# Kernel tuning notes

Hardware: AMD Instinct MI355X
Metric: run time of the kernel (lower is better)

Reference implementation:

```python
import jax, jax.numpy as jnp
import numpy as np

NEG_SLOPE = 0.01  # nn.LeakyReLU default


def setup_inputs() -> dict:
    key = jax.random.key(0)
    k1, k2, k3, k4, k5, k6 = jax.random.split(key, 6)
    N, E, F_IN, F_OUT = 50000, 800000, 256, 64
    x = jax.random.normal(k1, (N, F_IN), dtype=jnp.float32)
    src = jax.random.randint(k2, (E,), 0, N, dtype=jnp.int32)
    dst = jax.random.randint(k3, (E,), 0, N, dtype=jnp.int32)
    # nn.init.normal_(weight, 0, 0.5) for both Linear layers (no bias)
    W1 = 0.5 * jax.random.normal(k4, (F_OUT, F_IN), dtype=jnp.float32)
    W2 = 0.5 * jax.random.normal(k5, (F_OUT, F_OUT), dtype=jnp.float32)
    # detGAT.a = torch.rand(2*out_feats, 1)
    a = jax.random.uniform(k6, (2 * F_OUT, 1), dtype=jnp.float32)
    return {"x": x, "W1": W1, "W2": W2, "a": a, "src": src, "dst": dst}


def reference(x, W1, W2, a, src, dst):
    N, d = x.shape[0], W1.shape[0]
    # model_base: linear -> (dropout, identity in eval) -> relu, twice
    z = jax.nn.relu(x @ W1.T)
    h = jax.nn.relu(z @ W2.T)  # [N, d]
    # detGAT edge score: LeakyReLU(concat([h_dst, h_src]) @ a)
    # split a so we compute per-node dot products once instead of an [E, 2d] concat
    a_dst, a_src = a[:d, 0], a[d:, 0]
    s_dst = h @ a_dst  # [N]
    s_src = h @ a_src  # [N]
    score = jax.nn.leaky_relu(s_dst[dst] + s_src[src], NEG_SLOPE)  # [E]
    # edge_softmax: softmax over incoming edges of each destination node
    m = jax.ops.segment_max(score, dst, num_segments=N)  # [N]
    e = jnp.exp(score - m[dst])
    ssum = jax.ops.segment_sum(e, dst, num_segments=N)  # [N]
    w = e / ssum[dst]  # [E]
    # weighted scatter-sum of src features to dst nodes
    res = jax.ops.segment_sum(h[src] * w[:, None], dst, num_segments=N)  # [N, d]
    return jax.nn.relu(h - res)
```

## Files before the change

### kernel.cpp

```cpp
#include <hip/hip_runtime.h>
#include <math.h>

#define F_IN 256
#define F_OUT 64
#define NEG_SLOPE 0.01f
#define CAP 8192
#define NB2 256

typedef unsigned short ushort8_t __attribute__((ext_vector_type(8)));
typedef __bf16 bf16x8 __attribute__((ext_vector_type(8)));
typedef float f32x16 __attribute__((ext_vector_type(16)));

__device__ inline unsigned short f2bf(float f) {
    unsigned u = __float_as_uint(f);
    u += 0x7FFF + ((u >> 16) & 1);
    return (unsigned short)(u >> 16);
}
__device__ inline float bf2f(unsigned short u) {
    return __uint_as_float(((unsigned)u) << 16);
}
__device__ inline void splitbf(float x, unsigned short& hi, unsigned short& lo) {
    hi = f2bf(x);
    lo = f2bf(x - bf2f(hi));
}
__device__ inline bf16x8 asbf8(ushort8_t u) {
    union { ushort8_t u; bf16x8 b; } c; c.u = u; return c.b;
}
__device__ inline float redq32(float v) {
    v += __shfl_xor(v, 1);  v += __shfl_xor(v, 2);  v += __shfl_xor(v, 4);
    v += __shfl_xor(v, 8);  v += __shfl_xor(v, 16);
    return v;
}

__global__ __launch_bounds__(1024)
void prep_scatter_kernel(const float* __restrict__ W1, const float* __restrict__ W2,
                         unsigned short* __restrict__ w1fh, unsigned short* __restrict__ w1fl,
                         unsigned short* __restrict__ w2fh, unsigned short* __restrict__ w2fl,
                         const int* __restrict__ src, const int* __restrict__ dst,
                         int* __restrict__ cursor, int* __restrict__ edata,
                         int E, int chunk)
{
    __shared__ int lh[256], lbase[256], lcur[256];
    const int tid = threadIdx.x;

    if (blockIdx.x < 16) {
        int idx = blockIdx.x * 1024 + tid;
        int jj = idx & 7, l = (idx >> 3) & 63, t = idx >> 9;
        {
            int nt = t & 1, gks = t >> 1;
            int f = nt * 32 + (l & 31);
            int k = gks * 16 + (l >> 5) * 8 + jj;
            unsigned short hi, lo;
            splitbf(W1[f * F_IN + k], hi, lo);
            w1fh[idx] = hi; w1fl[idx] = lo;
        }
        if (idx < 4096) {
            int nt = t & 1, ks = t >> 1;
            int f = nt * 32 + (l & 31);
            int j = ks * 16 + (l >> 5) * 8 + jj;
            unsigned short hi, lo;
            splitbf(W2[f * F_OUT + j], hi, lo);
            w2fh[idx] = hi; w2fl[idx] = lo;
        }
        return;
    }

    const int bid = blockIdx.x - 16;
    if (tid < 256) lh[tid] = 0;
    __syncthreads();
    const int beg = bid * chunk;
    const int end = min(E, beg + chunk);
    for (int i = beg + tid; i < end; i += 1024)
        atomicAdd(&lh[((unsigned)dst[i]) >> 8], 1);
    __syncthreads();
    if (tid < 256) {
        int c = lh[tid];
        lbase[tid] = c ? atomicAdd(&cursor[tid], c) : 0;
        lcur[tid] = 0;
    }
    __syncthreads();
    for (int i = beg + tid; i < end; i += 1024) {
        int d = dst[i];
        int s = src[i];
        int b = ((unsigned)d) >> 8;
        int rk = atomicAdd(&lcur[b], 1);
        edata[b * CAP + lbase[b] + rk] = ((d & 0xFF) << 16) | s;
    }
}

__global__ __launch_bounds__(256, 2)
void mlp_kernel(const float* __restrict__ x,
                const unsigned short* __restrict__ w1fh,
                const unsigned short* __restrict__ w1fl,
                const unsigned short* __restrict__ w2fh,
                const unsigned short* __restrict__ w2fl,
                const float* __restrict__ a,
                unsigned short* __restrict__ hb,
                float* __restrict__ sdst,
                float* __restrict__ ssrc, int N)
{
    __shared__ __align__(16) unsigned short zbuf[4 * 8576];

    const int tid = threadIdx.x;
    const int lane = tid & 63;
    const int wid = __builtin_amdgcn_readfirstlane(tid >> 6);
    const int ml = lane & 31;
    const int q = lane >> 5;
    const int hl = lane >> 5;
    const int cl = lane & 31;
    const int node0w = blockIdx.x * 128 + wid * 32;

    unsigned short* xh = zbuf + wid * 8576;
    unsigned short* xl = xh + 4288;
    unsigned short* zh = xh;
    unsigned short* zl = xh + 2112;

    f32x16 acc0, acc1;
#pragma unroll
    for (int i = 0; i < 16; i++) { acc0[i] = 0.f; acc1[i] = 0.f; }

#pragma unroll
    for (int half = 0; half < 2; half++) {
        float4 v[16];
#pragma unroll
        for (int i = 0; i < 16; i++) {
            int r = 2 * i + hl;
            int rr = min(node0w + r, N - 1);
            v[i] = *(const float4*)(x + (size_t)rr * F_IN + half * 128 + cl * 4);
        }
#pragma unroll
        for (int i = 0; i < 16; i++) {
            int r = 2 * i + hl;
            ushort4 h4, l4;
            unsigned short th, tl;
            splitbf(v[i].x, th, tl); h4.x = th; l4.x = tl;
            splitbf(v[i].y, th, tl); h4.y = th; l4.y = tl;
            splitbf(v[i].z, th, tl); h4.z = th; l4.z = tl;
            splitbf(v[i].w, th, tl); h4.w = th; l4.w = tl;
            *(ushort4*)(xh + r * 134 + cl * 4) = h4;
            *(ushort4*)(xl + r * 134 + cl * 4) = l4;
        }
#pragma unroll
        for (int ks = 0; ks < 8; ks++) {
            int gks = half * 8 + ks;
            bf16x8 ah = asbf8(*(const ushort8_t*)(xh + ml * 134 + ks * 16 + q * 8));
            bf16x8 al = asbf8(*(const ushort8_t*)(xl + ml * 134 + ks * 16 + q * 8));
            bf16x8 bh0 = asbf8(*(const ushort8_t*)(w1fh + ((gks * 2 + 0) * 64 + lane) * 8));
            bf16x8 bl0 = asbf8(*(const ushort8_t*)(w1fl + ((gks * 2 + 0) * 64 + lane) * 8));
            bf16x8 bh1 = asbf8(*(const ushort8_t*)(w1fh + ((gks * 2 + 1) * 64 + lane) * 8));
            bf16x8 bl1 = asbf8(*(const ushort8_t*)(w1fl + ((gks * 2 + 1) * 64 + lane) * 8));
            acc0 = __builtin_amdgcn_mfma_f32_32x32x16_bf16(ah, bh0, acc0, 0, 0, 0);
            acc0 = __builtin_amdgcn_mfma_f32_32x32x16_bf16(ah, bl0, acc0, 0, 0, 0);
            acc0 = __builtin_amdgcn_mfma_f32_32x32x16_bf16(al, bh0, acc0, 0, 0, 0);
            acc1 = __builtin_amdgcn_mfma_f32_32x32x16_bf16(ah, bh1, acc1, 0, 0, 0);
            acc1 = __builtin_amdgcn_mfma_f32_32x32x16_bf16(ah, bl1, acc1, 0, 0, 0);
            acc1 = __builtin_amdgcn_mfma_f32_32x32x16_bf16(al, bh1, acc1, 0, 0, 0);
        }
    }

#pragma unroll
    for (int reg = 0; reg < 16; reg++) {
        int nd = (reg & 3) + 8 * (reg >> 2) + 4 * q;
        float z0 = fmaxf(acc0[reg], 0.f);
        float z1 = fmaxf(acc1[reg], 0.f);
        unsigned short h_, l_;
        splitbf(z0, h_, l_);
        zh[nd * 66 + ml] = h_; zl[nd * 66 + ml] = l_;
        splitbf(z1, h_, l_);
        zh[nd * 66 + 32 + ml] = h_; zl[nd * 66 + 32 + ml] = l_;
    }

    f32x16 hacc0, hacc1;
#pragma unroll
    for (int i = 0; i < 16; i++) { hacc0[i] = 0.f; hacc1[i] = 0.f; }
#pragma unroll
    for (int ks = 0; ks < 4; ks++) {
        bf16x8 wh0 = asbf8(*(const ushort8_t*)(w2fh + ((ks * 2 + 0) * 64 + lane) * 8));
        bf16x8 wl0 = asbf8(*(const ushort8_t*)(w2fl + ((ks * 2 + 0) * 64 + lane) * 8));
        bf16x8 wh1 = asbf8(*(const ushort8_t*)(w2fh + ((ks * 2 + 1) * 64 + lane) * 8));
        bf16x8 wl1 = asbf8(*(const ushort8_t*)(w2fl + ((ks * 2 + 1) * 64 + lane) * 8));
        bf16x8 ah = asbf8(*(const ushort8_t*)(zh + ml * 66 + ks * 16 + q * 8));
        bf16x8 al = asbf8(*(const ushort8_t*)(zl + ml * 66 + ks * 16 + q * 8));
        hacc0 = __builtin_amdgcn_mfma_f32_32x32x16_bf16(ah, wh0, hacc0, 0, 0, 0);
        hacc0 = __builtin_amdgcn_mfma_f32_32x32x16_bf16(ah, wl0, hacc0, 0, 0, 0);
        hacc0 = __builtin_amdgcn_mfma_f32_32x32x16_bf16(al, wh0, hacc0, 0, 0, 0);
        hacc1 = __builtin_amdgcn_mfma_f32_32x32x16_bf16(ah, wh1, hacc1, 0, 0, 0);
        hacc1 = __builtin_amdgcn_mfma_f32_32x32x16_bf16(ah, wl1, hacc1, 0, 0, 0);
        hacc1 = __builtin_amdgcn_mfma_f32_32x32x16_bf16(al, wh1, hacc1, 0, 0, 0);
    }

    const float aD0 = a[ml],            aD1 = a[32 + ml];
    const float aS0 = a[F_OUT + ml],    aS1 = a[F_OUT + 32 + ml];

    float sdv = 0.f, ssv = 0.f;
#pragma unroll
    for (int reg = 0; reg < 16; reg++) {
        int nd = (reg & 3) + 8 * (reg >> 2) + 4 * q;
        float h0 = fmaxf(hacc0[reg], 0.f);
        float h1 = fmaxf(hacc1[reg], 0.f);
        float td = redq32(h0 * aD0 + h1 * aD1);
        float ts = redq32(h0 * aS0 + h1 * aS1);
        if (ml == nd) { sdv = td; ssv = ts; }
        int gn = node0w + nd;
        if (gn < N) {
            hb[(size_t)gn * F_OUT + ml]      = f2bf(h0);
            hb[(size_t)gn * F_OUT + 32 + ml] = f2bf(h1);
        }
    }
    {
        int gn = node0w + ml;
        if ((((ml >> 2) & 1) == q) && gn < N) {
            sdst[gn] = sdv;
            ssrc[gn] = ssv;
        }
    }
}

__global__ __launch_bounds__(1024)
void sortagg_kernel(const int* __restrict__ cursor,
                    const int* __restrict__ edata,
                    const unsigned short* __restrict__ hb,
                    const float* __restrict__ sdst,
                    const float* __restrict__ ssrc,
                    float* __restrict__ out, int N)
{
    __shared__ int hist[256];
    __shared__ int excl[256];
    __shared__ int start_s[256];
    __shared__ unsigned short ssl[CAP];
    __shared__ float2 ws_sh[16][64];

    const int tid = threadIdx.x;
    const int lane = tid & 63;
    const int wid = tid >> 6;
    const int cb = blockIdx.x;
    const int base = cb * CAP;
    const int ecnt = cursor[cb];

    if (tid < 256) hist[tid] = 0;
    __syncthreads();
    for (int i = tid; i < ecnt; i += 1024)
        atomicAdd(&hist[((unsigned)edata[base + i]) >> 16], 1);
    __syncthreads();

    if (tid < 64) {
        int v0 = hist[lane * 4], v1 = hist[lane * 4 + 1];
        int v2 = hist[lane * 4 + 2], v3 = hist[lane * 4 + 3];
        int ts = v0 + v1 + v2 + v3;
        int s = ts;
#pragma unroll
        for (int d = 1; d < 64; d <<= 1) {
            int t = __shfl_up(s, d);
            if (lane >= d) s += t;
        }
        int e = s - ts;
        excl[lane * 4] = e;
        excl[lane * 4 + 1] = e + v0;
        excl[lane * 4 + 2] = e + v0 + v1;
        excl[lane * 4 + 3] = e + v0 + v1 + v2;
    }
    __syncthreads();
    if (tid < 256) start_s[tid] = excl[tid];
    __syncthreads();

    for (int i = tid; i < ecnt; i += 1024) {
        int pack = edata[base + i];
        int low = ((unsigned)pack) >> 16;
        int rk = atomicAdd(&excl[low], 1);
        ssl[rk] = (unsigned short)(pack & 0xFFFF);
    }
    __syncthreads();

    const int g = lane >> 4;
    const int li = lane & 15;
    const int grp = wid * 4 + g;

    for (int rep = 0; rep < 4; rep++) {
        const int local = rep * 64 + grp;
        const int d = cb * 256 + local;
        const bool vd = d < N;
        const int off = vd ? start_s[local] : 0;
        const int deg = vd ? hist[local] : 0;
        const float sdd = vd ? sdst[d] : 0.f;

        float M = -INFINITY, S = 0.f;
        float c0 = 0.f, c1 = 0.f, c2 = 0.f, c3 = 0.f;

        for (int ch = 0; ch < deg; ch += 16) {
            int ce = min(16, deg - ch);
            float score = -INFINITY;
            int s = 0;
            if (li < ce) {
                s = ssl[off + ch + li];
                float sc = sdd + ssrc[s];
                score = sc > 0.f ? sc : NEG_SLOPE * sc;
            }
            float mc = score;
            mc = fmaxf(mc, __shfl_xor(mc, 1));
            mc = fmaxf(mc, __shfl_xor(mc, 2));
            mc = fmaxf(mc, __shfl_xor(mc, 4));
            mc = fmaxf(mc, __shfl_xor(mc, 8));
            float newM = fmaxf(M, mc);
            float scale = __expf(M - newM);
            float w = (li < ce) ? __expf(score - newM) : 0.f;
            ws_sh[wid][lane] = make_float2(w, __int_as_float(s));
            float csum = w;
            csum += __shfl_xor(csum, 1);
            csum += __shfl_xor(csum, 2);
            csum += __shfl_xor(csum, 4);
            csum += __shfl_xor(csum, 8);
            S = S * scale + csum;
            __builtin_amdgcn_wave_barrier();

            float t0 = 0.f, t1 = 0.f, t2 = 0.f, t3 = 0.f;
#pragma unroll
            for (int e = 0; e < 16; e++) {
                float2 tw = ws_sh[wid][g * 16 + e];
                int se = __float_as_int(tw.y);
                ushort4 r = *(const ushort4*)(hb + (((size_t)(unsigned)se) << 6) + li * 4);
                t0 = fmaf(tw.x, bf2f(r.x), t0);
                t1 = fmaf(tw.x, bf2f(r.y), t1);
                t2 = fmaf(tw.x, bf2f(r.z), t2);
                t3 = fmaf(tw.x, bf2f(r.w), t3);
            }
            c0 = c0 * scale + t0;
            c1 = c1 * scale + t1;
            c2 = c2 * scale + t2;
            c3 = c3 * scale + t3;
            __builtin_amdgcn_wave_barrier();
            M = newM;
        }

        if (vd) {
            ushort4 hr = *(const ushort4*)(hb + (((size_t)(unsigned)d) << 6) + li * 4);
            float inv = (S > 0.f) ? 1.f / S : 0.f;
            float r0 = bf2f(hr.x) - c0 * inv;
            float r1 = bf2f(hr.y) - c1 * inv;
            float r2 = bf2f(hr.z) - c2 * inv;
            float r3 = bf2f(hr.w) - c3 * inv;
            float4 o;
            o.x = r0 > 0.f ? r0 : 0.f;
            o.y = r1 > 0.f ? r1 : 0.f;
            o.z = r2 > 0.f ? r2 : 0.f;
            o.w = r3 > 0.f ? r3 : 0.f;
            *(float4*)(out + (size_t)d * F_OUT + li * 4) = o;
        }
    }
}

extern "C" void kernel_launch(void* const* d_in, const int* in_sizes, int n_in,
                              void* d_out, int out_size, void* d_ws,
                              size_t ws_size, hipStream_t stream)
{
    const float* x  = (const float*)d_in[0];
    const float* W1 = (const float*)d_in[1];
    const float* W2 = (const float*)d_in[2];
    const float* a  = (const float*)d_in[3];
    const int* src  = (const int*)d_in[4];
    const int* dst  = (const int*)d_in[5];
    const int N = in_sizes[0] / F_IN;
    const int E = in_sizes[4];

    float* ws = (float*)d_ws;
    float* sdst = ws;
    float* ssrc = sdst + N;
    unsigned short* w1fh = (unsigned short*)(ssrc + N);
    unsigned short* w1fl = w1fh + 16384;
    unsigned short* w2fh = w1fl + 16384;
    unsigned short* w2fl = w2fh + 4096;
    unsigned short* hb = w2fl + 4096;
    int* cursor = (int*)(hb + (size_t)N * F_OUT);
    int* edata  = cursor + 256;

    const int nbc = (N + 255) >> 8;
    const int MLPB = (N + 127) >> 7;
    const int chunk = (E + NB2 - 1) / NB2;

    hipMemsetAsync(cursor, 0, 256 * sizeof(int), stream);
    prep_scatter_kernel<<<16 + NB2, 1024, 0, stream>>>(W1, W2, w1fh, w1fl, w2fh, w2fl,
                                                       src, dst, cursor, edata, E, chunk);
    mlp_kernel<<<MLPB, 256, 0, stream>>>(x, w1fh, w1fl, w2fh, w2fl, a,
                                         hb, sdst, ssrc, N);
    sortagg_kernel<<<nbc, 1024, 0, stream>>>(cursor, edata, hb, sdst, ssrc,
                                             (float*)d_out, N);
}
```

Before: 152.8 us.

## Switch MLP to 16x16x32 MFMA tiles with 16 nodes per wave

Reworks the MLP kernel to use 16x16x32 bf16 MFMAs instead of 32x32x16. Each wave now handles 16 nodes and each block 64 nodes, and the weight fragment layout in the prep kernel is rearranged to match. This halves the shared memory per block and raises the occupancy hint from 2 to 4 blocks, aiming for better latency hiding on the x loads. In exchange the grid has twice as many blocks, the weight fragments are reloaded per block, and there is a leftover redundant score expression.

```diff
diff --git a/kernel.cpp b/kernel.cpp
--- a/kernel.cpp
+++ b/kernel.cpp
@@ -9,7 +9,7 @@
 
 typedef unsigned short ushort8_t __attribute__((ext_vector_type(8)));
 typedef __bf16 bf16x8 __attribute__((ext_vector_type(8)));
-typedef float f32x16 __attribute__((ext_vector_type(16)));
+typedef float f32x4 __attribute__((ext_vector_type(4)));
 
 __device__ inline unsigned short f2bf(float f) {
     unsigned u = __float_as_uint(f);
@@ -25,11 +25,6 @@
 }
 __device__ inline bf16x8 asbf8(ushort8_t u) {
     union { ushort8_t u; bf16x8 b; } c; c.u = u; return c.b;
-}
-__device__ inline float redq32(float v) {
-    v += __shfl_xor(v, 1);  v += __shfl_xor(v, 2);  v += __shfl_xor(v, 4);
-    v += __shfl_xor(v, 8);  v += __shfl_xor(v, 16);
-    return v;
 }
 
 __global__ __launch_bounds__(1024)
@@ -45,21 +40,21 @@
 
     if (blockIdx.x < 16) {
         int idx = blockIdx.x * 1024 + tid;
-        int jj = idx & 7, l = (idx >> 3) & 63, t = idx >> 9;
+        int jj = idx & 7, l = (idx >> 3) & 63, u = idx >> 9;
         {
-            int nt = t & 1, gks = t >> 1;
-            int f = nt * 32 + (l & 31);
-            int k = gks * 16 + (l >> 5) * 8 + jj;
+            int gks = u >> 2, t = u & 3;
+            int f = t * 16 + (l & 15);
+            int k = gks * 32 + (l >> 4) * 8 + jj;
             unsigned short hi, lo;
             splitbf(W1[f * F_IN + k], hi, lo);
             w1fh[idx] = hi; w1fl[idx] = lo;
         }
         if (idx < 4096) {
-            int nt = t & 1, ks = t >> 1;
-            int f = nt * 32 + (l & 31);
-            int j = ks * 16 + (l >> 5) * 8 + jj;
+            int gks2 = u >> 2, t = u & 3;
+            int f = t * 16 + (l & 15);
+            int k = gks2 * 32 + (l >> 4) * 8 + jj;
             unsigned short hi, lo;
-            splitbf(W2[f * F_OUT + j], hi, lo);
+            splitbf(W2[f * F_OUT + k], hi, lo);
             w2fh[idx] = hi; w2fl[idx] = lo;
         }
         return;
@@ -88,7 +83,7 @@
     }
 }
 
-__global__ __launch_bounds__(256, 2)
+__global__ __launch_bounds__(256, 4)
 void mlp_kernel(const float* __restrict__ x,
                 const unsigned short* __restrict__ w1fh,
                 const unsigned short* __restrict__ w1fl,
@@ -99,119 +94,117 @@
                 float* __restrict__ sdst,
                 float* __restrict__ ssrc, int N)
 {
-    __shared__ __align__(16) unsigned short zbuf[4 * 8576];
+    __shared__ __align__(16) unsigned short zbuf[4 * 4288];
 
     const int tid = threadIdx.x;
     const int lane = tid & 63;
     const int wid = __builtin_amdgcn_readfirstlane(tid >> 6);
-    const int ml = lane & 31;
-    const int q = lane >> 5;
-    const int hl = lane >> 5;
-    const int cl = lane & 31;
-    const int node0w = blockIdx.x * 128 + wid * 32;
-
-    unsigned short* xh = zbuf + wid * 8576;
-    unsigned short* xl = xh + 4288;
+    const int m = lane & 15;
+    const int qq = lane >> 4;
+    const int node0w = blockIdx.x * 64 + wid * 16;
+
+    unsigned short* xh = zbuf + wid * 4288;
+    unsigned short* xl = xh + 2144;
     unsigned short* zh = xh;
-    unsigned short* zl = xh + 2112;
-
-    f32x16 acc0, acc1;
-#pragma unroll
-    for (int i = 0; i < 16; i++) { acc0[i] = 0.f; acc1[i] = 0.f; }
+    unsigned short* zl = xh + 1056 + 16;
+
+    f32x4 acc[4];
+#pragma unroll
+    for (int t = 0; t < 4; t++) acc[t] = (f32x4){0.f, 0.f, 0.f, 0.f};
 
 #pragma unroll
     for (int half = 0; half < 2; half++) {
-        float4 v[16];
-#pragma unroll
-        for (int i = 0; i < 16; i++) {
-            int r = 2 * i + hl;
+        float4 v[8];
+#pragma unroll
+        for (int i = 0; i < 8; i++) {
+            int r = i * 2 + (lane >> 5);
             int rr = min(node0w + r, N - 1);
-            v[i] = *(const float4*)(x + (size_t)rr * F_IN + half * 128 + cl * 4);
-        }
-#pragma unroll
-        for (int i = 0; i < 16; i++) {
-            int r = 2 * i + hl;
+            v[i] = *(const float4*)(x + (size_t)rr * F_IN + half * 128 + (lane & 31) * 4);
+        }
+#pragma unroll
+        for (int i = 0; i < 8; i++) {
+            int r = i * 2 + (lane >> 5);
             ushort4 h4, l4;
             unsigned short th, tl;
             splitbf(v[i].x, th, tl); h4.x = th; l4.x = tl;
             splitbf(v[i].y, th, tl); h4.y = th; l4.y = tl;
             splitbf(v[i].z, th, tl); h4.z = th; l4.z = tl;
             splitbf(v[i].w, th, tl); h4.w = th; l4.w = tl;
-            *(ushort4*)(xh + r * 134 + cl * 4) = h4;
-            *(ushort4*)(xl + r * 134 + cl * 4) = l4;
-        }
-#pragma unroll
-        for (int ks = 0; ks < 8; ks++) {
-            int gks = half * 8 + ks;
-            bf16x8 ah = asbf8(*(const ushort8_t*)(xh + ml * 134 + ks * 16 + q * 8));
-            bf16x8 al = asbf8(*(const ushort8_t*)(xl + ml * 134 + ks * 16 + q * 8));
-            bf16x8 bh0 = asbf8(*(const ushort8_t*)(w1fh + ((gks * 2 + 0) * 64 + lane) * 8));
-            bf16x8 bl0 = asbf8(*(const ushort8_t*)(w1fl + ((gks * 2 + 0) * 64 + lane) * 8));
-            bf16x8 bh1 = asbf8(*(const ushort8_t*)(w1fh + ((gks * 2 + 1) * 64 + lane) * 8));
-            bf16x8 bl1 = asbf8(*(const ushort8_t*)(w1fl + ((gks * 2 + 1) * 64 + lane) * 8));
-            acc0 = __builtin_amdgcn_mfma_f32_32x32x16_bf16(ah, bh0, acc0, 0, 0, 0);
-            acc0 = __builtin_amdgcn_mfma_f32_32x32x16_bf16(ah, bl0, acc0, 0, 0, 0);
-            acc0 = __builtin_amdgcn_mfma_f32_32x32x16_bf16(al, bh0, acc0, 0, 0, 0);
-            acc1 = __builtin_amdgcn_mfma_f32_32x32x16_bf16(ah, bh1, acc1, 0, 0, 0);
-            acc1 = __builtin_amdgcn_mfma_f32_32x32x16_bf16(ah, bl1, acc1, 0, 0, 0);
-            acc1 = __builtin_amdgcn_mfma_f32_32x32x16_bf16(al, bh1, acc1, 0, 0, 0);
-        }
-    }
-
-#pragma unroll
-    for (int reg = 0; reg < 16; reg++) {
-        int nd = (reg & 3) + 8 * (reg >> 2) + 4 * q;
-        float z0 = fmaxf(acc0[reg], 0.f);
-        float z1 = fmaxf(acc1[reg], 0.f);
-        unsigned short h_, l_;
-        splitbf(z0, h_, l_);
-        zh[nd * 66 + ml] = h_; zl[nd * 66 + ml] = l_;
-        splitbf(z1, h_, l_);
-        zh[nd * 66 + 32 + ml] = h_; zl[nd * 66 + 32 + ml] = l_;
-    }
-
-    f32x16 hacc0, hacc1;
-#pragma unroll
-    for (int i = 0; i < 16; i++) { hacc0[i] = 0.f; hacc1[i] = 0.f; }
-#pragma unroll
-    for (int ks = 0; ks < 4; ks++) {
-        bf16x8 wh0 = asbf8(*(const ushort8_t*)(w2fh + ((ks * 2 + 0) * 64 + lane) * 8));
-        bf16x8 wl0 = asbf8(*(const ushort8_t*)(w2fl + ((ks * 2 + 0) * 64 + lane) * 8));
-        bf16x8 wh1 = asbf8(*(const ushort8_t*)(w2fh + ((ks * 2 + 1) * 64 + lane) * 8));
-        bf16x8 wl1 = asbf8(*(const ushort8_t*)(w2fl + ((ks * 2 + 1) * 64 + lane) * 8));
-        bf16x8 ah = asbf8(*(const ushort8_t*)(zh + ml * 66 + ks * 16 + q * 8));
-        bf16x8 al = asbf8(*(const ushort8_t*)(zl + ml * 66 + ks * 16 + q * 8));
-        hacc0 = __builtin_amdgcn_mfma_f32_32x32x16_bf16(ah, wh0, hacc0, 0, 0, 0);
-        hacc0 = __builtin_amdgcn_mfma_f32_32x32x16_bf16(ah, wl0, hacc0, 0, 0, 0);
-        hacc0 = __builtin_amdgcn_mfma_f32_32x32x16_bf16(al, wh0, hacc0, 0, 0, 0);
-        hacc1 = __builtin_amdgcn_mfma_f32_32x32x16_bf16(ah, wh1, hacc1, 0, 0, 0);
-        hacc1 = __builtin_amdgcn_mfma_f32_32x32x16_bf16(ah, wl1, hacc1, 0, 0, 0);
-        hacc1 = __builtin_amdgcn_mfma_f32_32x32x16_bf16(al, wh1, hacc1, 0, 0, 0);
-    }
-
-    const float aD0 = a[ml],            aD1 = a[32 + ml];
-    const float aS0 = a[F_OUT + ml],    aS1 = a[F_OUT + 32 + ml];
-
-    float sdv = 0.f, ssv = 0.f;
-#pragma unroll
-    for (int reg = 0; reg < 16; reg++) {
-        int nd = (reg & 3) + 8 * (reg >> 2) + 4 * q;
-        float h0 = fmaxf(hacc0[reg], 0.f);
-        float h1 = fmaxf(hacc1[reg], 0.f);
-        float td = redq32(h0 * aD0 + h1 * aD1);
-        float ts = redq32(h0 * aS0 + h1 * aS1);
-        if (ml == nd) { sdv = td; ssv = ts; }
-        int gn = node0w + nd;
+            *(ushort4*)(xh + r * 134 + (lane & 31) * 4) = h4;
+            *(ushort4*)(xl + r * 134 + (lane & 31) * 4) = l4;
+        }
+#pragma unroll
+        for (int ksl = 0; ksl < 4; ksl++) {
+            int gks = half * 4 + ksl;
+            bf16x8 ah = asbf8(*(const ushort8_t*)(xh + m * 134 + ksl * 32 + qq * 8));
+            bf16x8 al = asbf8(*(const ushort8_t*)(xl + m * 134 + ksl * 32 + qq * 8));
+#pragma unroll
+            for (int t = 0; t < 4; t++) {
+                bf16x8 bh = asbf8(*(const ushort8_t*)(w1fh + ((gks * 4 + t) * 64 + lane) * 8));
+                bf16x8 bl = asbf8(*(const ushort8_t*)(w1fl + ((gks * 4 + t) * 64 + lane) * 8));
+                acc[t] = __builtin_amdgcn_mfma_f32_16x16x32_bf16(ah, bh, acc[t], 0, 0, 0);
+                acc[t] = __builtin_amdgcn_mfma_f32_16x16x32_bf16(ah, bl, acc[t], 0, 0, 0);
+                acc[t] = __builtin_amdgcn_mfma_f32_16x16x32_bf16(al, bh, acc[t], 0, 0, 0);
+            }
+        }
+    }
+
+#pragma unroll
+    for (int t = 0; t < 4; t++) {
+#pragma unroll
+        for (int reg = 0; reg < 4; reg++) {
+            int nd = qq * 4 + reg;
+            float z = fmaxf(acc[t][reg], 0.f);
+            unsigned short h_, l_;
+            splitbf(z, h_, l_);
+            zh[nd * 66 + t * 16 + m] = h_;
+            zl[nd * 66 + t * 16 + m] = l_;
+        }
+    }
+
+    f32x4 hacc[4];
+#pragma unroll
+    for (int t = 0; t < 4; t++) hacc[t] = (f32x4){0.f, 0.f, 0.f, 0.f};
+#pragma unroll
+    for (int ks2 = 0; ks2 < 2; ks2++) {
+        bf16x8 ah = asbf8(*(const ushort8_t*)(zh + m * 66 + ks2 * 32 + qq * 8));
+        bf16x8 al = asbf8(*(const ushort8_t*)(zl + m * 66 + ks2 * 32 + qq * 8));
+#pragma unroll
+        for (int t = 0; t < 4; t++) {
+            bf16x8 wh = asbf8(*(const ushort8_t*)(w2fh + ((ks2 * 4 + t) * 64 + lane) * 8));
+            bf16x8 wl = asbf8(*(const ushort8_t*)(w2fl + ((ks2 * 4 + t) * 64 + lane) * 8));
+            hacc[t] = __builtin_amdgcn_mfma_f32_16x16x32_bf16(ah, wh, hacc[t], 0, 0, 0);
+            hacc[t] = __builtin_amdgcn_mfma_f32_16x16x32_bf16(ah, wl, hacc[t], 0, 0, 0);
+            hacc[t] = __builtin_amdgcn_mfma_f32_16x16x32_bf16(al, wh, hacc[t], 0, 0, 0);
+        }
+    }
+
+    float aDv[4], aSv[4];
+#pragma unroll
+    for (int t = 0; t < 4; t++) {
+        aDv[t] = a[t * 16 + m];
+        aSv[t] = a[F_OUT + t * 16 + m];
+    }
+#pragma unroll
+    for (int reg = 0; reg < 4; reg++) {
+        float h0 = fmaxf(hacc[0][reg], 0.f);
+        float h1 = fmaxf(hacc[1][reg], 0.f);
+        float h2 = fmaxf(hacc[2][reg], 0.f);
+        float h3 = fmaxf(hacc[3][reg], 0.f);
+        float sd = h0 * aDv[0] + h1 * aSv[0] * 0.f + h1 * aDv[1] + h2 * aDv[2] + h3 * aDv[3];
+        sd = h0 * aDv[0] + h1 * aDv[1] + h2 * aDv[2] + h3 * aDv[3];
+        float ss = h0 * aSv[0] + h1 * aSv[1] + h2 * aSv[2] + h3 * aSv[3];
+        sd += __shfl_xor(sd, 1);  sd += __shfl_xor(sd, 2);
+        sd += __shfl_xor(sd, 4);  sd += __shfl_xor(sd, 8);
+        ss += __shfl_xor(ss, 1);  ss += __shfl_xor(ss, 2);
+        ss += __shfl_xor(ss, 4);  ss += __shfl_xor(ss, 8);
+        int gn = node0w + qq * 4 + reg;
         if (gn < N) {
-            hb[(size_t)gn * F_OUT + ml]      = f2bf(h0);
-            hb[(size_t)gn * F_OUT + 32 + ml] = f2bf(h1);
-        }
-    }
-    {
-        int gn = node0w + ml;
-        if ((((ml >> 2) & 1) == q) && gn < N) {
-            sdst[gn] = sdv;
-            ssrc[gn] = ssv;
+            hb[(size_t)gn * F_OUT +  0 + m] = f2bf(h0);
+            hb[(size_t)gn * F_OUT + 16 + m] = f2bf(h1);
+            hb[(size_t)gn * F_OUT + 32 + m] = f2bf(h2);
+            hb[(size_t)gn * F_OUT + 48 + m] = f2bf(h3);
+            if (m == reg) { sdst[gn] = sd; ssrc[gn] = ss; }
         }
     }
 }
@@ -373,7 +366,7 @@
     int* edata  = cursor + 256;
 
     const int nbc = (N + 255) >> 8;
-    const int MLPB = (N + 127) >> 7;
+    const int MLPB = (N + 63) >> 6;
     const int chunk = (E + NB2 - 1) / NB2;
 
     hipMemsetAsync(cursor, 0, 256 * sizeof(int), stream);
```

Result: faster. 148.7 us (-2.7%).
